# Performance work log

Measured on AMD Instinct MI355X. Metric: run time of the kernel, lower is better.

## Reference

```python
import jax, jax.numpy as jnp
import numpy as np

N, E = 50000, 800000
IN, HID, L, HEADS, OUT = 128, 256, 8, 8, 40
DH = HID // HEADS


def setup_inputs() -> dict:
    key = jax.random.key(0)
    ks = jax.random.split(key, 12)
    s = 0.05
    d = {}
    d["X"] = jax.random.normal(ks[0], (N, IN), jnp.float32)
    d["src"] = jax.random.randint(ks[1], (E,), 0, N, dtype=jnp.int32)
    d["dst"] = jax.random.randint(ks[2], (E,), 0, N, dtype=jnp.int32)
    d["Win"] = jax.random.normal(ks[3], (IN, HID), jnp.float32) * s
    d["bin_"] = jnp.zeros((HID,), jnp.float32)
    d["Wq"] = jax.random.normal(ks[4], (L, HID, HID), jnp.float32) * s
    d["Wk"] = jax.random.normal(ks[5], (L, HID, HID), jnp.float32) * s
    d["Wv"] = jax.random.normal(ks[6], (L, HID, HID), jnp.float32) * s
    d["bq"] = jnp.zeros((L, HID), jnp.float32)
    d["bk"] = jnp.zeros((L, HID), jnp.float32)
    d["bv"] = jnp.zeros((L, HID), jnp.float32)
    d["Wout"] = jax.random.normal(ks[7], (HID, OUT), jnp.float32) * s
    d["bout"] = jnp.zeros((OUT,), jnp.float32)
    return d


def _segment_softmax(e, seg, n):
    # e: [E, H] edge scores, seg: [E] destination node ids
    m = jax.ops.segment_max(e, seg, num_segments=n)
    ex = jnp.exp(e - m[seg])
    s = jax.ops.segment_sum(ex, seg, num_segments=n)
    return ex / s[seg]


def reference(X, src, dst, Win, bin_, Wq, Wk, Wv, bq, bk, bv, Wout, bout):
    n = X.shape[0]
    scaling = DH ** -0.5
    h = X @ Win + bin_  # in_proj: [N, HID]
    for l in range(L):  # fixed small layer stack
        q = (h @ Wq[l] + bq[l]).reshape(n, HEADS, DH) * scaling
        k = (h @ Wk[l] + bk[l]).reshape(n, HEADS, DH)
        v = (h @ Wv[l] + bv[l]).reshape(n, HEADS, DH)
        # SDDMM: per-edge, per-head dot product q[dst] . k[src]
        e = jnp.einsum('ehd,ehd->eh', q[dst], k[src])  # [E, HEADS]
        a = _segment_softmax(e, dst, n)                # softmax over in-edges of each dst
        # SpMM: weighted aggregation of source values into destinations
        h = jax.ops.segment_sum(a[..., None] * v[src], dst, num_segments=n).reshape(n, HID)
    return h @ Wout + bout  # predictor: [N, OUT]
```

## Files before the change

### kernel.cpp

```cpp
#include <hip/hip_runtime.h>
#include <hip/hip_bf16.h>
#include <hip/hip_fp16.h>

#define N_NODES 50000
#define MPAD    50048
#define N_EDGES 800000
#define IN_DIM  128
#define HID     256
#define QKVW    768
#define N_LAYERS 8
#define OUT_DIM 40
#define SCALING 0.17677669529663687f

typedef __attribute__((ext_vector_type(8))) _Float16 f16x8;
typedef __attribute__((ext_vector_type(4))) float f32x4;

__device__ __forceinline__ void gload_lds16(const void* g, void* l) {
    __builtin_amdgcn_global_load_lds(
        (__attribute__((address_space(1))) const unsigned int*)g,
        (__attribute__((address_space(3))) unsigned int*)l, 16, 0, 0);
}

__global__ void hist_kernel(const int* __restrict__ dst, int* __restrict__ cnt, int E) {
    int e = blockIdx.x * blockDim.x + threadIdx.x;
    if (e < E) atomicAdd(&cnt[dst[e]], 1);
}

__global__ __launch_bounds__(1024) void scan_kernel(const int* __restrict__ cnt,
                                                    int* __restrict__ row_off, int n) {
    __shared__ int wsum[16];
    __shared__ int carry_s;
    int tid = threadIdx.x;
    int lane = tid & 63, wid = tid >> 6;
    if (tid == 0) carry_s = 0;
    __syncthreads();
    for (int base = 0; base < n; base += 1024) {
        int i = base + tid;
        int x = (i < n) ? cnt[i] : 0;
        int v = x;
#pragma unroll
        for (int off = 1; off < 64; off <<= 1) {
            int y = __shfl_up(v, off);
            if (lane >= off) v += y;
        }
        if (lane == 63) wsum[wid] = v;
        __syncthreads();
        if (wid == 0) {
            int w = (lane < 16) ? wsum[lane] : 0;
#pragma unroll
            for (int off = 1; off < 16; off <<= 1) {
                int y = __shfl_up(w, off);
                if (lane >= off) w += y;
            }
            if (lane < 16) wsum[lane] = w;
        }
        __syncthreads();
        int wbase = (wid > 0) ? wsum[wid - 1] : 0;
        int carry = carry_s;
        if (i < n) row_off[i] = carry + wbase + v - x;
        int total = wsum[15];
        __syncthreads();
        if (tid == 0) carry_s = carry + total;
        __syncthreads();
    }
    if (tid == 0) row_off[n] = carry_s;
}

__global__ void scatter_kernel(const int* __restrict__ src, const int* __restrict__ dst,
                               const int* __restrict__ row_off, int* __restrict__ cur,
                               int* __restrict__ csr_src, int E) {
    int e = blockIdx.x * blockDim.x + threadIdx.x;
    if (e < E) {
        int d = dst[e];
        int pos = row_off[d] + atomicAdd(&cur[d], 1);
        csr_src[pos] = src[e];
    }
}

__global__ void wqkv_cvt_kernel(const float* __restrict__ Wq, const float* __restrict__ Wk,
                                const float* __restrict__ Wv, _Float16* __restrict__ outw) {
    int i = blockIdx.x * blockDim.x + threadIdx.x;
    if (i >= N_LAYERS * QKVW * HID) return;
    int k = i & 255;
    int n = (i >> 8) % QKVW;
    int l = i / (QKVW * HID);
    int seg = n >> 8, nn = n & 255;
    const float* W = (seg == 0) ? Wq : (seg == 1) ? Wk : Wv;
    outw[i] = (_Float16)W[((size_t)l * HID + k) * HID + nn];
}

__global__ void win_cvt_kernel(const float* __restrict__ Win, _Float16* __restrict__ outw) {
    int i = blockIdx.x * blockDim.x + threadIdx.x;
    if (i >= HID * IN_DIM) return;
    int k = i & 127;
    int n = i >> 7;
    outw[i] = (_Float16)Win[(size_t)k * HID + n];
}

__global__ void wout_cvt_kernel(const float* __restrict__ Wout, _Float16* __restrict__ hi,
                                _Float16* __restrict__ lo) {
    int i = blockIdx.x * blockDim.x + threadIdx.x;
    if (i >= 128 * HID) return;
    int k = i & 255;
    int n = i >> 8;
    float v = (n < OUT_DIM) ? Wout[(size_t)k * OUT_DIM + n] : 0.f;
    _Float16 h = (_Float16)v;
    hi[i] = h;
    lo[i] = (_Float16)(v - (float)h);
}

__global__ void x_cvt_kernel(const float* __restrict__ X, _Float16* __restrict__ outx) {
    int i = blockIdx.x * blockDim.x + threadIdx.x;
    if (i >= MPAD * IN_DIM) return;
    int r = i >> 7;
    outx[i] = (_Float16)((r < N_NODES) ? X[i] : 0.f);
}

template<int NT>
__global__ __launch_bounds__(256) void gemm16(
        const _Float16* __restrict__ A, const _Float16* __restrict__ B,
        const float* __restrict__ bias0, const float* __restrict__ bias1,
        const float* __restrict__ bias2, float scale0,
        _Float16* __restrict__ C, int ldC) {
    __shared__ __align__(16) _Float16 lds[2][2 * 4096];
    const int K = NT * 32;

    const int tid  = threadIdx.x;
    const int lane = tid & 63;
    const int wave = tid >> 6;
    const int row0 = blockIdx.x * 128;
    const int n0   = blockIdx.y * 128;

    const int p0 = wave * 64 + lane;
    const int p1 = p0 + 256;
    auto srcoff = [&](int p, int grow0) -> size_t {
        int row = p >> 2, cir = p & 3;
        int sw  = (row & 3) ^ ((row >> 2) & 3);
        int sc  = cir ^ sw;
        return (size_t)(grow0 + row) * K + sc * 8;
    };
    const size_t offA0 = srcoff(p0, row0), offA1 = srcoff(p1, row0);
    const size_t offB0 = srcoff(p0, n0),   offB1 = srcoff(p1, n0);
    const int d0 = wave * 512;
    const int d1 = 2048 + wave * 512;

    const int mh = (wave >> 1) * 64;
    const int nh = (wave & 1) * 64;
    int aoff[4], boff[4];
#pragma unroll
    for (int f = 0; f < 4; ++f) {
        int ra = mh + f * 16 + (lane & 15);
        int ca = (lane >> 4) ^ ((ra & 3) ^ ((ra >> 2) & 3));
        aoff[f] = ra * 64 + ca * 16;
        int rb = nh + f * 16 + (lane & 15);
        int cb = (lane >> 4) ^ ((rb & 3) ^ ((rb >> 2) & 3));
        boff[f] = rb * 64 + cb * 16;
    }

    f32x4 acc[4][4];
#pragma unroll
    for (int i = 0; i < 4; ++i)
#pragma unroll
        for (int j = 0; j < 4; ++j) acc[i][j] = {0.f, 0.f, 0.f, 0.f};

    auto STAGE = [&](int b, int t) {
        _Float16* LA = &lds[b][0];
        _Float16* LB = &lds[b][4096];
        const size_t k0 = (size_t)t * 32;
        gload_lds16(A + offA0 + k0, LA + d0);
        gload_lds16(A + offA1 + k0, LA + d1);
        gload_lds16(B + offB0 + k0, LB + d0);
        gload_lds16(B + offB1 + k0, LB + d1);
    };

    STAGE(0, 0);
#pragma unroll
    for (int t = 0; t < NT; ++t) {
        const int cur = t & 1;
        if (t + 1 < NT) {
            STAGE(cur ^ 1, t + 1);
            asm volatile("s_waitcnt vmcnt(4)" ::: "memory");
        } else {
            asm volatile("s_waitcnt vmcnt(0)" ::: "memory");
        }
        __builtin_amdgcn_s_barrier();
        const char* baseA = (const char*)&lds[cur][0];
        const char* baseB = (const char*)&lds[cur][4096];
        f16x8 af[4];
#pragma unroll
        for (int i = 0; i < 4; ++i)
            af[i] = *reinterpret_cast<const f16x8*>(baseA + aoff[i]);
#pragma unroll
        for (int j = 0; j < 4; ++j) {
            f16x8 bf = *reinterpret_cast<const f16x8*>(baseB + boff[j]);
#pragma unroll
            for (int i = 0; i < 4; ++i)
                acc[i][j] = __builtin_amdgcn_mfma_f32_16x16x32_f16(af[i], bf, acc[i][j], 0, 0, 0);
        }
        __builtin_amdgcn_s_barrier();
    }

    const int seg = n0 >> 8;
    const float* bias = (seg == 0) ? bias0 : (seg == 1) ? bias1 : bias2;
    const float scale = (seg == 0) ? scale0 : 1.f;
    const int fq = lane >> 4;
    const int fr = lane & 15;
#pragma unroll
    for (int i = 0; i < 4; ++i) {
#pragma unroll
        for (int j = 0; j < 4; ++j) {
#pragma unroll
            for (int r = 0; r < 4; ++r) {
                int m = row0 + mh + i * 16 + fq * 4 + r;
                int n = n0 + nh + j * 16 + fr;
                float o = (acc[i][j][r] + bias[n & 255]) * scale;
                C[(size_t)m * ldC + n] = (_Float16)o;
            }
        }
    }
}

__global__ __launch_bounds__(256) void gemm_out(
        const _Float16* __restrict__ A, const _Float16* __restrict__ Bh,
        const _Float16* __restrict__ Bl, const float* __restrict__ bias,
        float* __restrict__ C, int K) {
    __shared__ __align__(16) _Float16 lds[2][3 * 4096];

    const int tid  = threadIdx.x;
    const int lane = tid & 63;
    const int wave = tid >> 6;
    const int row0 = blockIdx.x * 128;

    const int p0 = wave * 64 + lane;
    const int p1 = p0 + 256;
    auto srcoff = [&](int p, int grow0) -> size_t {
        int row = p >> 2, cir = p & 3;
        int sw  = (row & 3) ^ ((row >> 2) & 3);
        int sc  = cir ^ sw;
        return (size_t)(grow0 + row) * K + sc * 8;
    };
    const size_t offA0 = srcoff(p0, row0), offA1 = srcoff(p1, row0);
    const size_t offB0 = srcoff(p0, 0),    offB1 = srcoff(p1, 0);
    const int d0 = wave * 512;
    const int d1 = 2048 + wave * 512;

    const int mh = (wave >> 1) * 64;
    const int nh = (wave & 1) * 64;
    int aoff[4], boff[4];
#pragma unroll
    for (int f = 0; f < 4; ++f) {
        int ra = mh + f * 16 + (lane & 15);
        int ca = (lane >> 4) ^ ((ra & 3) ^ ((ra >> 2) & 3));
        aoff[f] = ra * 64 + ca * 16;
        int rb = nh + f * 16 + (lane & 15);
        int cb = (lane >> 4) ^ ((rb & 3) ^ ((rb >> 2) & 3));
        boff[f] = rb * 64 + cb * 16;
    }

    f32x4 acc[4][4];
#pragma unroll
    for (int i = 0; i < 4; ++i)
#pragma unroll
        for (int j = 0; j < 4; ++j) acc[i][j] = {0.f, 0.f, 0.f, 0.f};

    auto STAGE = [&](int b, int t) {
        _Float16* LA  = &lds[b][0];
        _Float16* LBh = &lds[b][4096];
        _Float16* LBl = &lds[b][8192];
        const size_t k0 = (size_t)t * 32;
        gload_lds16(A  + offA0 + k0, LA  + d0);
        gload_lds16(A  + offA1 + k0, LA  + d1);
        gload_lds16(Bh + offB0 + k0, LBh + d0);
        gload_lds16(Bh + offB1 + k0, LBh + d1);
        gload_lds16(Bl + offB0 + k0, LBl + d0);
        gload_lds16(Bl + offB1 + k0, LBl + d1);
    };

    STAGE(0, 0);
#pragma unroll
    for (int t = 0; t < 8; ++t) {
        const int cur = t & 1;
        if (t + 1 < 8) {
            STAGE(cur ^ 1, t + 1);
            asm volatile("s_waitcnt vmcnt(6)" ::: "memory");
        } else {
            asm volatile("s_waitcnt vmcnt(0)" ::: "memory");
        }
        __builtin_amdgcn_s_barrier();
        const char* baseA  = (const char*)&lds[cur][0];
        const char* baseBh = (const char*)&lds[cur][4096];
        const char* baseBl = (const char*)&lds[cur][8192];
        f16x8 af[4];
#pragma unroll
        for (int i = 0; i < 4; ++i)
            af[i] = *reinterpret_cast<const f16x8*>(baseA + aoff[i]);
#pragma unroll
        for (int j = 0; j < 4; ++j) {
            f16x8 bh = *reinterpret_cast<const f16x8*>(baseBh + boff[j]);
            f16x8 bl = *reinterpret_cast<const f16x8*>(baseBl + boff[j]);
#pragma unroll
            for (int i = 0; i < 4; ++i) {
                acc[i][j] = __builtin_amdgcn_mfma_f32_16x16x32_f16(af[i], bh, acc[i][j], 0, 0, 0);
                acc[i][j] = __builtin_amdgcn_mfma_f32_16x16x32_f16(af[i], bl, acc[i][j], 0, 0, 0);
            }
        }
        __builtin_amdgcn_s_barrier();
    }

    const int fq = lane >> 4;
    const int fr = lane & 15;
#pragma unroll
    for (int i = 0; i < 4; ++i) {
#pragma unroll
        for (int j = 0; j < 4; ++j) {
#pragma unroll
            for (int r = 0; r < 4; ++r) {
                int m = row0 + mh + i * 16 + fq * 4 + r;
                int n = nh + j * 16 + fr;
                if (m < N_NODES && n < OUT_DIM)
                    C[(size_t)m * OUT_DIM + n] = acc[i][j][r] + bias[n];
            }
        }
    }
}

__global__ __launch_bounds__(256) void attn_kernel(
        const _Float16* __restrict__ qkv, const int* __restrict__ row_off,
        const int* __restrict__ csr_src, _Float16* __restrict__ h_out, int n) {
    int wave = threadIdx.x >> 6;
    int lane = threadIdx.x & 63;
    int node = blockIdx.x * 4 + wave;
    if (node >= n) return;
    const int loff = lane * 4;
    float4 qv;
    {
        float2 raw = *reinterpret_cast<const float2*>(&qkv[(size_t)node * QKVW + loff]);
        const __half2* h2 = reinterpret_cast<const __half2*>(&raw);
        float2 a = __half22float2(h2[0]), b = __half22float2(h2[1]);
        qv = make_float4(a.x, a.y, b.x, b.y);
    }
    float4 acc = make_float4(0.f, 0.f, 0.f, 0.f);
    float m = -INFINITY, s = 0.f;
    int beg = row_off[node], end = row_off[node + 1];
    int idx = beg;

#define LOAD_KV(slot, sn)                                                                 \
    float2 kr##slot, vr##slot;                                                            \
    {                                                                                     \
        const _Float16* base = qkv + (size_t)(sn) * QKVW;                                 \
        kr##slot = *reinterpret_cast<const float2*>(base + HID + loff);                   \
        vr##slot = *reinterpret_cast<const float2*>(base + 2 * HID + loff);               \
    }

#define DOT(slot, dvar)                                                                   \
    float dvar;                                                                           \
    {                                                                                     \
        const __half2* kh = reinterpret_cast<const __half2*>(&kr##slot);                  \
        float2 k01 = __half22float2(kh[0]), k23 = __half22float2(kh[1]);                  \
        dvar = qv.x * k01.x + qv.y * k01.y + qv.z * k23.x + qv.w * k23.y;                 \
        dvar += __shfl_xor(dvar, 1);                                                      \
        dvar += __shfl_xor(dvar, 2);                                                      \
        dvar += __shfl_xor(dvar, 4);                                                      \
    }

#define VADD(slot, p)                                                                     \
    {                                                                                     \
        const __half2* vh = reinterpret_cast<const __half2*>(&vr##slot);                  \
        float2 v01 = __half22float2(vh[0]), v23 = __half22float2(vh[1]);                  \
        acc.x = fmaf(p, v01.x, acc.x);                                                    \
        acc.y = fmaf(p, v01.y, acc.y);                                                    \
        acc.z = fmaf(p, v23.x, acc.z);                                                    \
        acc.w = fmaf(p, v23.y, acc.w);                                                    \
    }

    for (; idx + 3 < end; idx += 4) {
        int s0 = csr_src[idx], s1 = csr_src[idx + 1];
        int s2 = csr_src[idx + 2], s3 = csr_src[idx + 3];
        LOAD_KV(0, s0) LOAD_KV(1, s1) LOAD_KV(2, s2) LOAD_KV(3, s3)
        DOT(0, e0) DOT(1, e1) DOT(2, e2) DOT(3, e3)
        float mn = fmaxf(fmaxf(fmaxf(m, e0), fmaxf(e1, e2)), e3);
        float c  = __expf(m - mn);
        float p0 = __expf(e0 - mn), p1 = __expf(e1 - mn);
        float p2 = __expf(e2 - mn), p3 = __expf(e3 - mn);
        s = fmaf(s, c, (p0 + p1) + (p2 + p3));
        acc.x *= c; acc.y *= c; acc.z *= c; acc.w *= c;
        VADD(0, p0) VADD(1, p1) VADD(2, p2) VADD(3, p3)
        m = mn;
    }
    for (; idx < end; ++idx) {
        int s0 = csr_src[idx];
        LOAD_KV(0, s0)
        DOT(0, e0)
        float mn = fmaxf(m, e0);
        float c = __expf(m - mn);
        float p0 = __expf(e0 - mn);
        s = fmaf(s, c, p0);
        acc.x *= c; acc.y *= c; acc.z *= c; acc.w *= c;
        VADD(0, p0)
        m = mn;
    }
#undef LOAD_KV
#undef DOT
#undef VADD

    float inv = (s > 0.f) ? 1.f / s : 0.f;
    __half2 o01 = __floats2half2_rn(acc.x * inv, acc.y * inv);
    __half2 o23 = __floats2half2_rn(acc.z * inv, acc.w * inv);
    union { __half2 h2[2]; float2 f2; } u;
    u.h2[0] = o01; u.h2[1] = o23;
    *reinterpret_cast<float2*>(&h_out[(size_t)node * HID + loff]) = u.f2;
}

extern "C" void kernel_launch(void* const* d_in, const int* in_sizes, int n_in,
                              void* d_out, int out_size, void* d_ws, size_t ws_size,
                              hipStream_t stream) {
    const float* X    = (const float*)d_in[0];
    const int*   src  = (const int*)d_in[1];
    const int*   dst  = (const int*)d_in[2];
    const float* Win  = (const float*)d_in[3];
    const float* bin_ = (const float*)d_in[4];
    const float* Wq   = (const float*)d_in[5];
    const float* Wk   = (const float*)d_in[6];
    const float* Wv   = (const float*)d_in[7];
    const float* bq   = (const float*)d_in[8];
    const float* bk   = (const float*)d_in[9];
    const float* bv   = (const float*)d_in[10];
    const float* Wout = (const float*)d_in[11];
    const float* bout = (const float*)d_in[12];
    float* out = (float*)d_out;

    char* ws = (char*)d_ws;
    size_t off = 0;
    auto alloc = [&](size_t bytes) -> void* {
        void* p = ws + off;
        off = (off + bytes + 255) & ~(size_t)255;
        return p;
    };
    _Float16* qkv   = (_Float16*)alloc((size_t)MPAD * QKVW * 2);
    _Float16* h     = (_Float16*)alloc((size_t)MPAD * HID * 2);
    _Float16* Xf    = (_Float16*)alloc((size_t)MPAD * IN_DIM * 2);
    _Float16* Wqkvt = (_Float16*)alloc((size_t)N_LAYERS * QKVW * HID * 2);
    _Float16* Wint  = (_Float16*)alloc((size_t)HID * IN_DIM * 2);
    _Float16* Wot_h = (_Float16*)alloc((size_t)128 * HID * 2);
    _Float16* Wot_l = (_Float16*)alloc((size_t)128 * HID * 2);
    int* cnt     = (int*)alloc(sizeof(int) * N_NODES);
    int* row_off = (int*)alloc(sizeof(int) * (N_NODES + 1));
    int* csr_src = (int*)alloc(sizeof(int) * N_EDGES);

    hipMemsetAsync(cnt, 0, sizeof(int) * N_NODES, stream);
    hist_kernel<<<(N_EDGES + 255) / 256, 256, 0, stream>>>(dst, cnt, N_EDGES);
    scan_kernel<<<1, 1024, 0, stream>>>(cnt, row_off, N_NODES);
    hipMemsetAsync(cnt, 0, sizeof(int) * N_NODES, stream);
    scatter_kernel<<<(N_EDGES + 255) / 256, 256, 0, stream>>>(src, dst, row_off, cnt, csr_src, N_EDGES);

    {
        int t1 = N_LAYERS * QKVW * HID;
        wqkv_cvt_kernel<<<(t1 + 255) / 256, 256, 0, stream>>>(Wq, Wk, Wv, Wqkvt);
        int t2 = HID * IN_DIM;
        win_cvt_kernel<<<(t2 + 255) / 256, 256, 0, stream>>>(Win, Wint);
        int t3 = 128 * HID;
        wout_cvt_kernel<<<(t3 + 255) / 256, 256, 0, stream>>>(Wout, Wot_h, Wot_l);
        int t4 = MPAD * IN_DIM;
        x_cvt_kernel<<<(t4 + 255) / 256, 256, 0, stream>>>(X, Xf);
    }

    dim3 blk(256);
    gemm16<4><<<dim3(MPAD / 128, 2), blk, 0, stream>>>(
        Xf, Wint, bin_, bin_, bin_, 1.f, h, HID);

    for (int l = 0; l < N_LAYERS; ++l) {
        const _Float16* Bl = Wqkvt + (size_t)l * QKVW * HID;
        gemm16<8><<<dim3(MPAD / 128, 6), blk, 0, stream>>>(
            h, Bl, bq + l * HID, bk + l * HID, bv + l * HID, SCALING, qkv, QKVW);
        attn_kernel<<<(N_NODES + 3) / 4, blk, 0, stream>>>(
            qkv, row_off, csr_src, h, N_NODES);
    }
    gemm_out<<<dim3(MPAD / 128, 1), blk, 0, stream>>>(
        h, Wot_h, Wot_l, bout, out, HID);
}
```

Before: 1.518 ms.

## Double-buffer neighbor K/V loads in attention and remap GEMM block order

In the attention kernel, the next group of four neighbors' K/V loads is issued before the current group is processed, using two register sets, so gather latency overlaps with the softmax and accumulate work. The GEMM grid is flattened to 1D and block indices are remapped so that eight consecutive row blocks are grouped and all column tiles of a row group are scheduled close together. This is meant to improve L2 reuse of A rows, and possibly to spread blocks across XCDs. The cost is higher register pressure in the attention kernel and a few idle padded blocks in the GEMM.

```diff
diff --git a/kernel.cpp b/kernel.cpp
--- a/kernel.cpp
+++ b/kernel.cpp
@@ -4,6 +4,7 @@
 
 #define N_NODES 50000
 #define MPAD    50048
+#define NRB     391
 #define N_EDGES 800000
 #define IN_DIM  128
 #define HID     256
@@ -116,7 +117,7 @@
     outx[i] = (_Float16)((r < N_NODES) ? X[i] : 0.f);
 }
 
-template<int NT>
+template<int NT, int NCOLT>
 __global__ __launch_bounds__(256) void gemm16(
         const _Float16* __restrict__ A, const _Float16* __restrict__ B,
         const float* __restrict__ bias0, const float* __restrict__ bias1,
@@ -125,11 +126,17 @@
     __shared__ __align__(16) _Float16 lds[2][2 * 4096];
     const int K = NT * 32;
 
+    const int bb = blockIdx.x;
+    const int xx = bb & 7, tt = bb >> 3;
+    const int qq = tt / NCOLT, jj = tt - qq * NCOLT;
+    const int rowblk = qq * 8 + xx;
+    if (rowblk >= NRB) return;
+    const int row0 = rowblk * 128;
+    const int n0   = jj * 128;
+
     const int tid  = threadIdx.x;
     const int lane = tid & 63;
     const int wave = tid >> 6;
-    const int row0 = blockIdx.x * 128;
-    const int n0   = blockIdx.y * 128;
 
     const int p0 = wave * 64 + lane;
     const int p1 = p0 + 256;
@@ -322,6 +329,24 @@
             }
         }
     }
+}
+
+__device__ __forceinline__ float edot(const float4& qv, const float2& kr) {
+    const __half2* kh = reinterpret_cast<const __half2*>(&kr);
+    float2 k01 = __half22float2(kh[0]), k23 = __half22float2(kh[1]);
+    float d = qv.x * k01.x + qv.y * k01.y + qv.z * k23.x + qv.w * k23.y;
+    d += __shfl_xor(d, 1);
+    d += __shfl_xor(d, 2);
+    d += __shfl_xor(d, 4);
+    return d;
+}
+__device__ __forceinline__ void vadd(float4& acc, float p, const float2& vr) {
+    const __half2* vh = reinterpret_cast<const __half2*>(&vr);
+    float2 v01 = __half22float2(vh[0]), v23 = __half22float2(vh[1]);
+    acc.x = fmaf(p, v01.x, acc.x);
+    acc.y = fmaf(p, v01.y, acc.y);
+    acc.z = fmaf(p, v23.x, acc.z);
+    acc.w = fmaf(p, v23.y, acc.w);
 }
 
 __global__ __launch_bounds__(256) void attn_kernel(
@@ -344,64 +369,75 @@
     int beg = row_off[node], end = row_off[node + 1];
     int idx = beg;
 
-#define LOAD_KV(slot, sn)                                                                 \
-    float2 kr##slot, vr##slot;                                                            \
+    float2 kA0, kA1, kA2, kA3, vA0, vA1, vA2, vA3;
+    float2 kB0, kB1, kB2, kB3, vB0, vB1, vB2, vB3;
+
+#define ISSUE(S, i0)                                                                      \
     {                                                                                     \
-        const _Float16* base = qkv + (size_t)(sn) * QKVW;                                 \
-        kr##slot = *reinterpret_cast<const float2*>(base + HID + loff);                   \
-        vr##slot = *reinterpret_cast<const float2*>(base + 2 * HID + loff);               \
-    }
-
-#define DOT(slot, dvar)                                                                   \
-    float dvar;                                                                           \
+        int t0 = csr_src[(i0)], t1 = csr_src[(i0) + 1];                                   \
+        int t2 = csr_src[(i0) + 2], t3 = csr_src[(i0) + 3];                               \
+        const _Float16* b0 = qkv + (size_t)t0 * QKVW;                                     \
+        const _Float16* b1 = qkv + (size_t)t1 * QKVW;                                     \
+        const _Float16* b2 = qkv + (size_t)t2 * QKVW;                                     \
+        const _Float16* b3 = qkv + (size_t)t3 * QKVW;                                     \
+        k##S##0 = *(const float2*)(b0 + HID + loff);                                      \
+        v##S##0 = *(const float2*)(b0 + 2 * HID + loff);                                  \
+        k##S##1 = *(const float2*)(b1 + HID + loff);                                      \
+        v##S##1 = *(const float2*)(b1 + 2 * HID + loff);                                  \
+        k##S##2 = *(const float2*)(b2 + HID + loff);                                      \
+        v##S##2 = *(const float2*)(b2 + 2 * HID + loff);                                  \
+        k##S##3 = *(const float2*)(b3 + HID + loff);                                      \
+        v##S##3 = *(const float2*)(b3 + 2 * HID + loff);                                  \
+    }
+
+#define PROCESS(S)                                                                        \
     {                                                                                     \
-        const __half2* kh = reinterpret_cast<const __half2*>(&kr##slot);                  \
-        float2 k01 = __half22float2(kh[0]), k23 = __half22float2(kh[1]);                  \
-        dvar = qv.x * k01.x + qv.y * k01.y + qv.z * k23.x + qv.w * k23.y;                 \
-        dvar += __shfl_xor(dvar, 1);                                                      \
-        dvar += __shfl_xor(dvar, 2);                                                      \
-        dvar += __shfl_xor(dvar, 4);                                                      \
-    }
-
-#define VADD(slot, p)                                                                     \
-    {                                                                                     \
-        const __half2* vh = reinterpret_cast<const __half2*>(&vr##slot);                  \
-        float2 v01 = __half22float2(vh[0]), v23 = __half22float2(vh[1]);                  \
-        acc.x = fmaf(p, v01.x, acc.x);                                                    \
-        acc.y = fmaf(p, v01.y, acc.y);                                                    \
-        acc.z = fmaf(p, v23.x, acc.z);                                                    \
-        acc.w = fmaf(p, v23.y, acc.w);                                                    \
-    }
-
-    for (; idx + 3 < end; idx += 4) {
-        int s0 = csr_src[idx], s1 = csr_src[idx + 1];
-        int s2 = csr_src[idx + 2], s3 = csr_src[idx + 3];
-        LOAD_KV(0, s0) LOAD_KV(1, s1) LOAD_KV(2, s2) LOAD_KV(3, s3)
-        DOT(0, e0) DOT(1, e1) DOT(2, e2) DOT(3, e3)
-        float mn = fmaxf(fmaxf(fmaxf(m, e0), fmaxf(e1, e2)), e3);
-        float c  = __expf(m - mn);
-        float p0 = __expf(e0 - mn), p1 = __expf(e1 - mn);
-        float p2 = __expf(e2 - mn), p3 = __expf(e3 - mn);
-        s = fmaf(s, c, (p0 + p1) + (p2 + p3));
-        acc.x *= c; acc.y *= c; acc.z *= c; acc.w *= c;
-        VADD(0, p0) VADD(1, p1) VADD(2, p2) VADD(3, p3)
-        m = mn;
+        float e0 = edot(qv, k##S##0), e1 = edot(qv, k##S##1);                             \
+        float e2 = edot(qv, k##S##2), e3 = edot(qv, k##S##3);                             \
+        float mn = fmaxf(fmaxf(fmaxf(m, e0), fmaxf(e1, e2)), e3);                         \
+        float c  = __expf(m - mn);                                                        \
+        float p0 = __expf(e0 - mn), p1 = __expf(e1 - mn);                                 \
+        float p2 = __expf(e2 - mn), p3 = __expf(e3 - mn);                                 \
+        s = fmaf(s, c, (p0 + p1) + (p2 + p3));                                            \
+        acc.x *= c; acc.y *= c; acc.z *= c; acc.w *= c;                                   \
+        vadd(acc, p0, v##S##0); vadd(acc, p1, v##S##1);                                   \
+        vadd(acc, p2, v##S##2); vadd(acc, p3, v##S##3);                                   \
+        m = mn;                                                                           \
+    }
+
+    if (idx + 3 < end) {
+        ISSUE(A, idx);
+        while (true) {
+            int nxt = idx + 4;
+            bool haveB = (nxt + 3 < end);
+            if (haveB) ISSUE(B, nxt);
+            PROCESS(A);
+            idx = nxt;
+            if (!haveB) break;
+            nxt = idx + 4;
+            bool haveA = (nxt + 3 < end);
+            if (haveA) ISSUE(A, nxt);
+            PROCESS(B);
+            idx = nxt;
+            if (!haveA) break;
+        }
     }
     for (; idx < end; ++idx) {
         int s0 = csr_src[idx];
-        LOAD_KV(0, s0)
-        DOT(0, e0)
+        const _Float16* base = qkv + (size_t)s0 * QKVW;
+        float2 kr = *(const float2*)(base + HID + loff);
+        float2 vr = *(const float2*)(base + 2 * HID + loff);
+        float e0 = edot(qv, kr);
         float mn = fmaxf(m, e0);
         float c = __expf(m - mn);
         float p0 = __expf(e0 - mn);
         s = fmaf(s, c, p0);
         acc.x *= c; acc.y *= c; acc.z *= c; acc.w *= c;
-        VADD(0, p0)
+        vadd(acc, p0, vr);
         m = mn;
     }
-#undef LOAD_KV
-#undef DOT
-#undef VADD
+#undef ISSUE
+#undef PROCESS
 
     float inv = (s > 0.f) ? 1.f / s : 0.f;
     __half2 o01 = __floats2half2_rn(acc.x * inv, acc.y * inv);
@@ -465,16 +501,17 @@
     }
 
     dim3 blk(256);
-    gemm16<4><<<dim3(MPAD / 128, 2), blk, 0, stream>>>(
+    const int NQ = 8 * ((NRB + 7) / 8);
+    gemm16<4, 2><<<dim3(NQ * 2), blk, 0, stream>>>(
         Xf, Wint, bin_, bin_, bin_, 1.f, h, HID);
 
     for (int l = 0; l < N_LAYERS; ++l) {
         const _Float16* Bl = Wqkvt + (size_t)l * QKVW * HID;
-        gemm16<8><<<dim3(MPAD / 128, 6), blk, 0, stream>>>(
+        gemm16<8, 6><<<dim3(NQ * 6), blk, 0, stream>>>(
             h, Bl, bq + l * HID, bk + l * HID, bv + l * HID, SCALING, qkv, QKVW);
         attn_kernel<<<(N_NODES + 3) / 4, blk, 0, stream>>>(
             qkv, row_off, csr_src, h, N_NODES);
     }
-    gemm_out<<<dim3(MPAD / 128, 1), blk, 0, stream>>>(
+    gemm_out<<<dim3(NRB), blk, 0, stream>>>(
         h, Wot_h, Wot_l, bout, out, HID);
 }
```

Result: faster. 1.435 ms (-5.5%).

## Triple-buffer GEMM LDS pipeline and remap blocks for XCD-aware L2 locality

Applied to the files above, without the earlier changes.

Raises GEMM LDS staging from two buffers to three, keeping two K-tiles of global-to-LDS loads in flight, with adjusted vmcnt waits. The 2D grid becomes a 1D grid whose block index is decoded so that groups of 8 consecutive blocks (one per XCD) cover different row blocks while the column tiles of a row block share an XCD, aiming to improve L2 reuse of the A rows. CSR construction drops one memset by giving the scatter pass its own zeroed counter array. More LDS per block may lower occupancy, and padded blocks exit early.

```diff
diff --git a/kernel.cpp b/kernel.cpp
--- a/kernel.cpp
+++ b/kernel.cpp
@@ -4,6 +4,7 @@
 
 #define N_NODES 50000
 #define MPAD    50048
+#define NRB     391
 #define N_EDGES 800000
 #define IN_DIM  128
 #define HID     256
@@ -116,20 +117,26 @@
     outx[i] = (_Float16)((r < N_NODES) ? X[i] : 0.f);
 }
 
-template<int NT>
+template<int NT, int NCOLT>
 __global__ __launch_bounds__(256) void gemm16(
         const _Float16* __restrict__ A, const _Float16* __restrict__ B,
         const float* __restrict__ bias0, const float* __restrict__ bias1,
         const float* __restrict__ bias2, float scale0,
         _Float16* __restrict__ C, int ldC) {
-    __shared__ __align__(16) _Float16 lds[2][2 * 4096];
+    __shared__ __align__(16) _Float16 lds[3][2 * 4096];
     const int K = NT * 32;
+
+    const int bb = blockIdx.x;
+    const int xx = bb & 7, tt = bb >> 3;
+    const int qq = tt / NCOLT, jj = tt - qq * NCOLT;
+    const int rowblk = qq * 8 + xx;
+    if (rowblk >= NRB) return;
+    const int row0 = rowblk * 128;
+    const int n0   = jj * 128;
 
     const int tid  = threadIdx.x;
     const int lane = tid & 63;
     const int wave = tid >> 6;
-    const int row0 = blockIdx.x * 128;
-    const int n0   = blockIdx.y * 128;
 
     const int p0 = wave * 64 + lane;
     const int p1 = p0 + 256;
@@ -174,18 +181,20 @@
     };
 
     STAGE(0, 0);
+    STAGE(1, 1);
 #pragma unroll
     for (int t = 0; t < NT; ++t) {
-        const int cur = t & 1;
-        if (t + 1 < NT) {
-            STAGE(cur ^ 1, t + 1);
+        if (t + 2 < NT) {
+            STAGE((t + 2) % 3, t + 2);
+            asm volatile("s_waitcnt vmcnt(8)" ::: "memory");
+        } else if (t + 1 < NT) {
             asm volatile("s_waitcnt vmcnt(4)" ::: "memory");
         } else {
             asm volatile("s_waitcnt vmcnt(0)" ::: "memory");
         }
         __builtin_amdgcn_s_barrier();
-        const char* baseA = (const char*)&lds[cur][0];
-        const char* baseB = (const char*)&lds[cur][4096];
+        const char* baseA = (const char*)&lds[t % 3][0];
+        const char* baseB = (const char*)&lds[t % 3][4096];
         f16x8 af[4];
 #pragma unroll
         for (int i = 0; i < 4; ++i)
@@ -224,7 +233,7 @@
         const _Float16* __restrict__ A, const _Float16* __restrict__ Bh,
         const _Float16* __restrict__ Bl, const float* __restrict__ bias,
         float* __restrict__ C, int K) {
-    __shared__ __align__(16) _Float16 lds[2][3 * 4096];
+    __shared__ __align__(16) _Float16 lds[3][3 * 4096];
 
     const int tid  = threadIdx.x;
     const int lane = tid & 63;
@@ -277,19 +286,21 @@
     };
 
     STAGE(0, 0);
+    STAGE(1, 1);
 #pragma unroll
     for (int t = 0; t < 8; ++t) {
-        const int cur = t & 1;
-        if (t + 1 < 8) {
-            STAGE(cur ^ 1, t + 1);
+        if (t + 2 < 8) {
+            STAGE((t + 2) % 3, t + 2);
+            asm volatile("s_waitcnt vmcnt(12)" ::: "memory");
+        } else if (t + 1 < 8) {
             asm volatile("s_waitcnt vmcnt(6)" ::: "memory");
         } else {
             asm volatile("s_waitcnt vmcnt(0)" ::: "memory");
         }
         __builtin_amdgcn_s_barrier();
-        const char* baseA  = (const char*)&lds[cur][0];
-        const char* baseBh = (const char*)&lds[cur][4096];
-        const char* baseBl = (const char*)&lds[cur][8192];
+        const char* baseA  = (const char*)&lds[t % 3][0];
+        const char* baseBh = (const char*)&lds[t % 3][4096];
+        const char* baseBl = (const char*)&lds[t % 3][8192];
         f16x8 af[4];
 #pragma unroll
         for (int i = 0; i < 4; ++i)
@@ -443,15 +454,15 @@
     _Float16* Wint  = (_Float16*)alloc((size_t)HID * IN_DIM * 2);
     _Float16* Wot_h = (_Float16*)alloc((size_t)128 * HID * 2);
     _Float16* Wot_l = (_Float16*)alloc((size_t)128 * HID * 2);
-    int* cnt     = (int*)alloc(sizeof(int) * N_NODES);
+    int* cnt     = (int*)alloc(sizeof(int) * 2 * N_NODES);
     int* row_off = (int*)alloc(sizeof(int) * (N_NODES + 1));
     int* csr_src = (int*)alloc(sizeof(int) * N_EDGES);
 
-    hipMemsetAsync(cnt, 0, sizeof(int) * N_NODES, stream);
+    hipMemsetAsync(cnt, 0, sizeof(int) * 2 * N_NODES, stream);
     hist_kernel<<<(N_EDGES + 255) / 256, 256, 0, stream>>>(dst, cnt, N_EDGES);
     scan_kernel<<<1, 1024, 0, stream>>>(cnt, row_off, N_NODES);
-    hipMemsetAsync(cnt, 0, sizeof(int) * N_NODES, stream);
-    scatter_kernel<<<(N_EDGES + 255) / 256, 256, 0, stream>>>(src, dst, row_off, cnt, csr_src, N_EDGES);
+    scatter_kernel<<<(N_EDGES + 255) / 256, 256, 0, stream>>>(src, dst, row_off,
+                                                              cnt + N_NODES, csr_src, N_EDGES);
 
     {
         int t1 = N_LAYERS * QKVW * HID;
@@ -465,16 +476,17 @@
     }
 
     dim3 blk(256);
-    gemm16<4><<<dim3(MPAD / 128, 2), blk, 0, stream>>>(
+    const int NQ = 8 * ((NRB + 7) / 8);
+    gemm16<4, 2><<<dim3(NQ * 2), blk, 0, stream>>>(
         Xf, Wint, bin_, bin_, bin_, 1.f, h, HID);
 
     for (int l = 0; l < N_LAYERS; ++l) {
         const _Float16* Bl = Wqkvt + (size_t)l * QKVW * HID;
-        gemm16<8><<<dim3(MPAD / 128, 6), blk, 0, stream>>>(
+        gemm16<8, 6><<<dim3(NQ * 6), blk, 0, stream>>>(
             h, Bl, bq + l * HID, bk + l * HID, bv + l * HID, SCALING, qkv, QKVW);
         attn_kernel<<<(N_NODES + 3) / 4, blk, 0, stream>>>(
             qkv, row_off, csr_src, h, N_NODES);
     }
-    gemm_out<<<dim3(MPAD / 128, 1), blk, 0, stream>>>(
+    gemm_out<<<dim3(NRB), blk, 0, stream>>>(
         h, Wot_h, Wot_l, bout, out, HID);
 }
```

Measured after the change: 1.422 ms. -6.3%, faster.
